# Performance work log

Hardware: AMD Instinct MI355X
Metric: run time of the kernel (lower is better)

Reference implementation:

```python
import math
import jax, jax.numpy as jnp
import numpy as np

B, NQ, NK, DIM, H, HD = 2, 1024, 2048, 1024, 16, 64


def setup_inputs() -> dict:
    key = jax.random.key(0)
    ks = jax.random.split(key, 12)
    s = 1.0 / math.sqrt(DIM)
    return {
        "q": jax.random.normal(ks[0], (B, NQ, DIM), jnp.float32),
        "k": jax.random.normal(ks[1], (B, NK, DIM), jnp.float32),
        "v": jax.random.normal(ks[2], (B, NK, DIM), jnp.float32),
        "distances": jax.random.uniform(ks[3], (B, NQ, NK), jnp.float32),
        "attn_mask": jax.random.bernoulli(ks[4], 0.5, (B, NQ, NK)),
        "key_padding_mask_q": jax.random.bernoulli(ks[5], 0.5, (B, NQ)),
        "key_padding_mask_k": jax.random.bernoulli(ks[6], 0.5, (B, NK)),
        "Wq": jax.random.normal(ks[7], (H * HD, DIM), jnp.float32) * s,
        "Wk": jax.random.normal(ks[8], (H * HD, DIM), jnp.float32) * s,
        "Wv": jax.random.normal(ks[9], (H * HD, DIM), jnp.float32) * s,
        "Wo": jax.random.normal(ks[10], (DIM, H * HD), jnp.float32) * s,
        "gate_alpha": jnp.float32(0.1),
    }


def reference(q, k, v, distances, attn_mask, key_padding_mask_q,
              key_padding_mask_k, Wq, Wk, Wv, Wo, gate_alpha):
    bsz, q_len, _ = q.shape
    k_len = k.shape[1]
    neg = jnp.finfo(q.dtype).min

    # projections -> (B, H, N, HD)
    qp = (q @ Wq.T).reshape(bsz, q_len, H, HD).transpose(0, 2, 1, 3)
    kp = (k @ Wk.T).reshape(bsz, k_len, H, HD).transpose(0, 2, 1, 3)
    vp = (v @ Wv.T).reshape(bsz, k_len, H, HD).transpose(0, 2, 1, 3)

    scores = jnp.einsum('bhqd,bhkd->bhqk', qp, kp) / math.sqrt(HD)
    scores = jnp.where(attn_mask[:, None, :, :], scores, neg)
    scores = jnp.where(key_padding_mask_k[:, None, None, :], scores, neg)

    attn = jax.nn.softmax(scores, axis=-1)  # (B,H,NQ,NK)

    # distance gating: mask, batch-mean normalize, exponential gate
    d = distances * attn_mask.astype(distances.dtype)
    d = d * key_padding_mask_k[:, None, :].astype(d.dtype)
    mean = d.sum(axis=(-1, -2)) / (q_len * k_len + 1e-6)
    mean = jnp.maximum(mean, 1e-6)[:, None, None]
    d = d / mean
    alpha = jax.nn.softplus(gate_alpha)
    gate = jnp.exp(-alpha * d)[:, None, :, :]  # (B,1,NQ,NK)

    w = attn * gate
    w = w / (w.sum(axis=-1, keepdims=True) + 1e-6)

    out = jnp.einsum('bhqk,bhkd->bhqd', w, vp)
    out = out.transpose(0, 2, 1, 3).reshape(bsz, q_len, H * HD)
    out = out * key_padding_mask_q[:, :, None].astype(out.dtype)
    return out @ Wo.T
```

## Files before the change

kernel.cpp:

```cpp
#include <hip/hip_runtime.h>
#include <hip/hip_bf16.h>
#include <cfloat>

#define B_   2
#define NQ_  1024
#define NK_  2048
#define H_   16
#define HD_  64
#define VPAD 2176
#define GPAD 2112

typedef float  floatx4 __attribute__((ext_vector_type(4)));
typedef __bf16 bf16x8  __attribute__((ext_vector_type(8)));
typedef __bf16 bf16x4  __attribute__((ext_vector_type(4)));

static __device__ __forceinline__ floatx4 mfma16(bf16x8 a, bf16x8 b, floatx4 c) {
    return __builtin_amdgcn_mfma_f32_16x16x32_bf16(a, b, c, 0, 0, 0);
}

static __device__ __forceinline__ void gl_lds(const __bf16* g, __bf16* lbase,
                                              int lane) {
#if __has_builtin(__builtin_amdgcn_global_load_lds)
    __builtin_amdgcn_global_load_lds(
        (const __attribute__((address_space(1))) void*)g,
        (__attribute__((address_space(3))) void*)lbase, 16, 0, 0);
#else
    *(bf16x8*)(lbase + lane * 8) = *(const bf16x8*)g;
#endif
}

struct CvtArgs {
    const float* src[7];
    __bf16*      dst[7];
};

__global__ __launch_bounds__(256) void cvt_mean_kernel(
    CvtArgs a, const float* __restrict__ dist, const int* __restrict__ amask,
    const int* __restrict__ kpmk, float* __restrict__ msum,
    __bf16* __restrict__ dmask)
{
    if (blockIdx.x >= 1792) {
        const int mb = blockIdx.x - 1792;
        const int b  = mb >> 9;
        const float* d  = dist  + (size_t)b * NQ_ * NK_;
        const int*   am = amask + (size_t)b * NQ_ * NK_;
        const int*   km = kpmk  + b * NK_;
        __bf16*      dm = dmask + (size_t)b * NQ_ * GPAD;
        const int base = (mb & 511) * 256 + threadIdx.x;
        float s = 0.f;
        #pragma unroll
        for (int j = 0; j < 4; j++) {
            const int i   = base + j * 131072;
            const int idx = i * 4;
            const int kk  = idx & (NK_ - 1);
            const int q   = i >> 9;
            float4 dv = *(const float4*)(d + idx);
            int4   mv = *(const int4*)(am + idx);
            int4   kv = *(const int4*)(km + kk);
            bf16x4 o;
            if (mv.x && kv.x) { s += dv.x; o[0] = (__bf16)dv.x; } else o[0] = (__bf16)3e38f;
            if (mv.y && kv.y) { s += dv.y; o[1] = (__bf16)dv.y; } else o[1] = (__bf16)3e38f;
            if (mv.z && kv.z) { s += dv.z; o[2] = (__bf16)dv.z; } else o[2] = (__bf16)3e38f;
            if (mv.w && kv.w) { s += dv.w; o[3] = (__bf16)dv.w; } else o[3] = (__bf16)3e38f;
            *(bf16x4*)&dm[(size_t)q * GPAD + kk] = o;
        }
        #pragma unroll
        for (int off = 32; off >= 1; off >>= 1) s += __shfl_down(s, off);
        __shared__ float wsum[4];
        if ((threadIdx.x & 63) == 0) wsum[threadIdx.x >> 6] = s;
        __syncthreads();
        if (threadIdx.x == 0)
            atomicAdd(&msum[b], wsum[0] + wsum[1] + wsum[2] + wsum[3]);
        return;
    }
    #pragma unroll
    for (int j = 0; j < 4; j++) {
        size_t r = (size_t)blockIdx.x * 1024 + j * 256 + threadIdx.x;
        int s;
        if (r < 262144)                  { s = 0; }
        else if ((r -= 262144) < 524288) { s = 1; }
        else if ((r -= 524288) < 524288) { s = 2; }
        else { r -= 524288; s = 3 + (int)(r >> 17); r &= 131071; }
        const float* sp = a.src[s] + r * 8;
        float4 f0 = *(const float4*)sp;
        float4 f1 = *(const float4*)(sp + 4);
        bf16x8 o;
        o[0] = (__bf16)f0.x; o[1] = (__bf16)f0.y; o[2] = (__bf16)f0.z; o[3] = (__bf16)f0.w;
        o[4] = (__bf16)f1.x; o[5] = (__bf16)f1.y; o[6] = (__bf16)f1.z; o[7] = (__bf16)f1.w;
        *(bf16x8*)(a.dst[s] + r * 8) = o;
    }
}

template <typename EPI>
static __device__ __forceinline__ void gemm128_core(
    const __bf16* __restrict__ A, const __bf16* __restrict__ Bw,
    int m0, int n0, __bf16* As, __bf16* Bs, EPI epi)
{
    const int t    = threadIdx.x;
    const int w    = t >> 6, lane = t & 63;
    const int lrow = lane & 15, quad = lane >> 4;
    const int lr   = lane >> 2, lc = lane & 3;

    floatx4 acc[4][4];
    #pragma unroll
    for (int mi = 0; mi < 4; mi++)
        #pragma unroll
        for (int ni = 0; ni < 4; ni++) acc[mi][ni] = floatx4{0.f, 0.f, 0.f, 0.f};

    const __bf16* ga = A  + (size_t)(m0 + w * 32 + lr) * 1024 + lc * 8;
    const __bf16* gb = Bw + (size_t)(n0 + w * 32 + lr) * 1024 + lc * 8;

    for (int k0 = 0; k0 < 1024; k0 += 64) {
        __syncthreads();
        #pragma unroll
        for (int h = 0; h < 2; h++) {
            gl_lds(ga + k0 + h * 32,             &As[h * 4096 + (w * 32) * 32],      lane);
            gl_lds(ga + k0 + h * 32 + 16 * 1024, &As[h * 4096 + (w * 32 + 16) * 32], lane);
            gl_lds(gb + k0 + h * 32,             &Bs[h * 4096 + (w * 32) * 32],      lane);
            gl_lds(gb + k0 + h * 32 + 16 * 1024, &Bs[h * 4096 + (w * 32 + 16) * 32], lane);
        }
        __syncthreads();

        #pragma unroll
        for (int h = 0; h < 2; h++) {
            bf16x8 af[4], bfr[4];
            #pragma unroll
            for (int mi = 0; mi < 4; mi++)
                af[mi] = *(const bf16x8*)
                    &As[h * 4096 + ((w & 1) * 64 + mi * 16 + lrow) * 32 + quad * 8];
            #pragma unroll
            for (int ni = 0; ni < 4; ni++)
                bfr[ni] = *(const bf16x8*)
                    &Bs[h * 4096 + ((w >> 1) * 64 + ni * 16 + lrow) * 32 + quad * 8];
            #pragma unroll
            for (int mi = 0; mi < 4; mi++)
                #pragma unroll
                for (int ni = 0; ni < 4; ni++)
                    acc[mi][ni] = mfma16(af[mi], bfr[ni], acc[mi][ni]);
        }
    }

    #pragma unroll
    for (int mi = 0; mi < 4; mi++)
        #pragma unroll
        for (int ni = 0; ni < 4; ni++)
            #pragma unroll
            for (int r = 0; r < 4; r++) {
                const int m = m0 + (w & 1) * 64 + mi * 16 + quad * 4 + r;
                const int n = n0 + (w >> 1) * 64 + ni * 16 + lrow;
                epi(m, n, acc[mi][ni][r]);
            }
}

__global__ __launch_bounds__(256) void proj_kernel(
    const __bf16* __restrict__ qb, const __bf16* __restrict__ kb,
    const __bf16* __restrict__ vb, const __bf16* __restrict__ wqb,
    const __bf16* __restrict__ wkb, const __bf16* __restrict__ wvb,
    __bf16* __restrict__ qp, __bf16* __restrict__ kp,
    __bf16* __restrict__ vpT)
{
    __shared__ alignas(16) __bf16 As[2 * 128 * 32];
    __shared__ alignas(16) __bf16 Bs[2 * 128 * 32];
    const int z = blockIdx.z;
    if (z == 0) {
        if ((int)blockIdx.x >= 16) return;
        gemm128_core(qb, wqb, blockIdx.x * 128, blockIdx.y * 128, As, Bs,
                     [&](int m, int n, float v) {
            const int b = m >> 10, q = m & 1023;
            const int h = n >> 6,  d = n & 63;
            qp[(((size_t)(b * 16 + h) * NQ_ + q) << 6) + d] = (__bf16)v;
        });
    } else if (z == 1) {
        gemm128_core(kb, wkb, blockIdx.x * 128, blockIdx.y * 128, As, Bs,
                     [&](int m, int n, float v) {
            const int b = m >> 11, key = m & 2047;
            const int h = n >> 6,  d = n & 63;
            kp[(((size_t)(b * 16 + h) * NK_ + key) << 6) + d] = (__bf16)v;
        });
    } else {
        gemm128_core(wvb, vb, blockIdx.y * 128, blockIdx.x * 128, As, Bs,
                     [&](int m, int n, float v) {
            const int h = m >> 6,  d = m & 63;
            const int b = n >> 11, key = n & 2047;
            vpT[((size_t)(b * 16 + h) * HD_ + d) * VPAD + key] = (__bf16)v;
        });
    }
}

__global__ __launch_bounds__(512) void oproj_kernel(
    const __bf16* __restrict__ A, const __bf16* __restrict__ W,
    float* __restrict__ Cout)
{
    __shared__ alignas(16) __bf16 As[2][64 * 32];
    __shared__ alignas(16) __bf16 Bs[2][128 * 32];
    const int t    = threadIdx.x;
    const int w    = t >> 6, lane = t & 63;
    const int lrow = lane & 15, quad = lane >> 4;
    const int lr   = lane >> 2, lc = lane & 3;
    const int m0 = blockIdx.x * 64, n0 = blockIdx.y * 128;
    const int wm = w & 1, wn = w >> 1;

    floatx4 acc[2][2];
    #pragma unroll
    for (int mi = 0; mi < 2; mi++)
        #pragma unroll
        for (int ni = 0; ni < 2; ni++) acc[mi][ni] = floatx4{0.f, 0.f, 0.f, 0.f};

    const __bf16* ga = A + (size_t)(m0 + (w & 3) * 16 + lr) * 1024 + lc * 8;
    const __bf16* gb = W + (size_t)(n0 + w * 16 + lr) * 1024 + lc * 8;

    for (int k0 = 0; k0 < 1024; k0 += 64) {
        __syncthreads();
        #pragma unroll
        for (int h = 0; h < 2; h++) {
            if (w < 4)
                gl_lds(ga + k0 + h * 32, &As[h][(w * 16) * 32], lane);
            gl_lds(gb + k0 + h * 32, &Bs[h][(w * 16) * 32], lane);
        }
        __syncthreads();

        #pragma unroll
        for (int h = 0; h < 2; h++) {
            bf16x8 af[2], bfr[2];
            #pragma unroll
            for (int mi = 0; mi < 2; mi++)
                af[mi] = *(const bf16x8*)
                    &As[h][(wm * 32 + mi * 16 + lrow) * 32 + quad * 8];
            #pragma unroll
            for (int ni = 0; ni < 2; ni++)
                bfr[ni] = *(const bf16x8*)
                    &Bs[h][(wn * 32 + ni * 16 + lrow) * 32 + quad * 8];
            #pragma unroll
            for (int mi = 0; mi < 2; mi++)
                #pragma unroll
                for (int ni = 0; ni < 2; ni++)
                    acc[mi][ni] = mfma16(af[mi], bfr[ni], acc[mi][ni]);
        }
    }

    #pragma unroll
    for (int mi = 0; mi < 2; mi++)
        #pragma unroll
        for (int ni = 0; ni < 2; ni++)
            #pragma unroll
            for (int r = 0; r < 4; r++) {
                const int m = m0 + wm * 32 + mi * 16 + quad * 4 + r;
                const int n = n0 + wn * 32 + ni * 16 + lrow;
                Cout[(size_t)m * 1024 + n] = acc[mi][ni][r];
            }
}

__global__ __launch_bounds__(256, 2) void attn_kernel(
    const __bf16* __restrict__ qp, const __bf16* __restrict__ kp,
    const __bf16* __restrict__ vpT, const __bf16* __restrict__ dmask,
    const float* __restrict__ msum, const float* __restrict__ galpha,
    float* __restrict__ Opart, float* __restrict__ Gpart)
{
    __shared__ __bf16 Ks[64 * 72];
    __shared__ __bf16 Vt[2][64 * 72];
    __shared__ __bf16 Ps[4][32 * 72];
    const int t    = threadIdx.x;
    const int w    = t >> 6, lane = t & 63;
    const int lrow = lane & 15, quad = lane >> 4;
    const int bid  = ((blockIdx.x & 7) << 6) | (blockIdx.x >> 3);
    const int qt   = bid & 7;
    const int bh   = (bid >> 3) & 31;
    const int z    = bid >> 8;
    const int b    = bh >> 4, h = bh & 15;
    const int q0   = qt * 128 + w * 32;
    const int kb0  = z * (NK_ / 2);
    const int NT   = NK_ / 128;

    const float mean  = fmaxf(msum[b] / ((float)(NQ_ * NK_) + 1e-6f), 1e-6f);
    const float alpha = log1pf(__expf(galpha[0]));
    const float cg    = -alpha / mean;

    bf16x8 qf0[2], qf1[2];
    #pragma unroll
    for (int g = 0; g < 2; g++) {
        const __bf16* qb = qp + ((size_t)bh * NQ_ + q0 + g * 16 + lrow) * HD_
                         + quad * 8;
        qf0[g] = *(const bf16x8*)qb;
        qf1[g] = *(const bf16x8*)(qb + 32);
    }

    const int srow0 = t >> 3,        sc0 = t & 7;
    const int srow1 = 32 + (t >> 3), sc1 = t & 7;
    const int so0 = srow0 * 72 + sc0 * 8;
    const int so1 = srow1 * 72 + sc1 * 8;
    const __bf16* Kg = kp  + ((size_t)bh * NK_ + kb0) * HD_;
    const __bf16* Vg = vpT + (size_t)bh * HD_ * VPAD + kb0;
    const __bf16* grow0 = dmask + ((size_t)b * NQ_ + q0 + lrow) * GPAD + kb0;
    const __bf16* grow1 = grow0 + (size_t)16 * GPAD;

    float G[2] = {0.f, 0.f};
    floatx4 O[2][4];
    #pragma unroll
    for (int g = 0; g < 2; g++)
        #pragma unroll
        for (int nb = 0; nb < 4; nb++) O[g][nb] = floatx4{0.f, 0.f, 0.f, 0.f};

    bf16x8 kr0, kr1, vr0, vr1;
    bf16x4 gr[2][4];
    auto loadt = [&](int kb) {
        kr0 = *(const bf16x8*)(Kg + (size_t)(kb + srow0) * HD_ + sc0 * 8);
        kr1 = *(const bf16x8*)(Kg + (size_t)(kb + srow1) * HD_ + sc1 * 8);
        vr0 = *(const bf16x8*)(Vg + (size_t)srow0 * VPAD + kb + sc0 * 8);
        vr1 = *(const bf16x8*)(Vg + (size_t)srow1 * VPAD + kb + sc1 * 8);
        #pragma unroll
        for (int c = 0; c < 4; c++) {
            gr[0][c] = *(const bf16x4*)(grow0 + kb + c * 16 + quad * 4);
            gr[1][c] = *(const bf16x4*)(grow1 + kb + c * 16 + quad * 4);
        }
    };
    loadt(0);

    for (int ib = 0; ib < NT; ib++) {
        const int kb  = ib * 64;
        const int cur = ib & 1;

        __syncthreads();
        *(bf16x8*)&Ks[so0]      = kr0;
        *(bf16x8*)&Ks[so1]      = kr1;
        *(bf16x8*)&Vt[cur][so0] = vr0;
        *(bf16x8*)&Vt[cur][so1] = vr1;
        __syncthreads();

        bf16x4 gcur[2][4];
        #pragma unroll
        for (int g = 0; g < 2; g++)
            #pragma unroll
            for (int c = 0; c < 4; c++) gcur[g][c] = gr[g][c];
        if (ib + 1 < NT) loadt(kb + 64);

        __builtin_amdgcn_s_setprio(1);
        floatx4 s4[2][4];
        #pragma unroll
        for (int c = 0; c < 4; c++) {
            bf16x8 kf0 = *(const bf16x8*)&Ks[(c * 16 + lrow) * 72 + quad * 8];
            bf16x8 kf1 = *(const bf16x8*)&Ks[(c * 16 + lrow) * 72 + 32 + quad * 8];
            #pragma unroll
            for (int g = 0; g < 2; g++) {
                floatx4 a = floatx4{0.f, 0.f, 0.f, 0.f};
                a = mfma16(kf0, qf0[g], a);
                a = mfma16(kf1, qf1[g], a);
                s4[g][c] = a;
            }
        }

        if (ib > 0) {
            const int prv = cur ^ 1;
            bf16x8 pf0[2], pf1[2];
            #pragma unroll
            for (int g = 0; g < 2; g++) {
                pf0[g] = *(const bf16x8*)&Ps[w][(g * 16 + lrow) * 72 + quad * 8];
                pf1[g] = *(const bf16x8*)&Ps[w][(g * 16 + lrow) * 72 + 32 + quad * 8];
            }
            #pragma unroll
            for (int nb = 0; nb < 4; nb++) {
                bf16x8 vf0 = *(const bf16x8*)
                    &Vt[prv][(nb * 16 + lrow) * 72 + quad * 8];
                bf16x8 vf1 = *(const bf16x8*)
                    &Vt[prv][(nb * 16 + lrow) * 72 + 32 + quad * 8];
                #pragma unroll
                for (int g = 0; g < 2; g++) {
                    O[g][nb] = mfma16(pf0[g], vf0, O[g][nb]);
                    O[g][nb] = mfma16(pf1[g], vf1, O[g][nb]);
                }
            }
        }
        __builtin_amdgcn_s_setprio(0);

        #pragma unroll
        for (int g = 0; g < 2; g++)
            #pragma unroll
            for (int c = 0; c < 4; c++) {
                const float e0 = __expf(fmaf(s4[g][c][0], 0.125f, cg * (float)gcur[g][c][0]));
                const float e1 = __expf(fmaf(s4[g][c][1], 0.125f, cg * (float)gcur[g][c][1]));
                const float e2 = __expf(fmaf(s4[g][c][2], 0.125f, cg * (float)gcur[g][c][2]));
                const float e3 = __expf(fmaf(s4[g][c][3], 0.125f, cg * (float)gcur[g][c][3]));
                G[g] += (e0 + e1) + (e2 + e3);
                bf16x4 pk;
                pk[0] = (__bf16)e0; pk[1] = (__bf16)e1;
                pk[2] = (__bf16)e2; pk[3] = (__bf16)e3;
                *(bf16x4*)&Ps[w][(g * 16 + lrow) * 72 + c * 16 + quad * 4] = pk;
            }
    }

    {
        const int prv = (NT - 1) & 1;
        bf16x8 pf0[2], pf1[2];
        #pragma unroll
        for (int g = 0; g < 2; g++) {
            pf0[g] = *(const bf16x8*)&Ps[w][(g * 16 + lrow) * 72 + quad * 8];
            pf1[g] = *(const bf16x8*)&Ps[w][(g * 16 + lrow) * 72 + 32 + quad * 8];
        }
        #pragma unroll
        for (int nb = 0; nb < 4; nb++) {
            bf16x8 vf0 = *(const bf16x8*)&Vt[prv][(nb * 16 + lrow) * 72 + quad * 8];
            bf16x8 vf1 = *(const bf16x8*)&Vt[prv][(nb * 16 + lrow) * 72 + 32 + quad * 8];
            #pragma unroll
            for (int g = 0; g < 2; g++) {
                O[g][nb] = mfma16(pf0[g], vf0, O[g][nb]);
                O[g][nb] = mfma16(pf1[g], vf1, O[g][nb]);
            }
        }
    }

    #pragma unroll
    for (int g = 0; g < 2; g++) {
        G[g] += __shfl_xor(G[g], 16);
        G[g] += __shfl_xor(G[g], 32);
    }

    #pragma unroll
    for (int g = 0; g < 2; g++) {
        float* Op = Opart + (size_t)z * (B_ * NQ_ * 1024)
                          + ((size_t)b * NQ_ + q0 + g * 16) * 1024 + h * HD_;
        #pragma unroll
        for (int r = 0; r < 4; r++) {
            const int qr = quad * 4 + r;
            #pragma unroll
            for (int nb = 0; nb < 4; nb++)
                Op[(size_t)qr * 1024 + nb * 16 + lrow] = O[g][nb][r];
        }
        if (lane < 16)
            Gpart[(size_t)z * (32 * 1024) + bh * 1024 + q0 + g * 16 + lane] = G[g];
    }
}

__global__ __launch_bounds__(256) void combine_kernel(
    const float* __restrict__ Opart, const float* __restrict__ Gpart,
    const int* __restrict__ kpmq, __bf16* __restrict__ attnout)
{
    const int idx = blockIdx.x * 256 + threadIdx.x;
    const int m   = idx >> 8;
    const int c4  = (idx & 255) * 4;
    const int b   = m >> 10, q = m & 1023;
    const int h   = c4 >> 6;
    const float g = Gpart[(b * 16 + h) * 1024 + q]
                  + Gpart[32 * 1024 + (b * 16 + h) * 1024 + q];
    const float f = kpmq[b * NQ_ + q] ? 1.f / (g + 1e-30f) : 0.f;
    const float4 o0 = *(const float4*)(Opart + (size_t)m * 1024 + c4);
    const float4 o1 = *(const float4*)(Opart + (size_t)(B_ * NQ_) * 1024
                                              + (size_t)m * 1024 + c4);
    bf16x4 r;
    r[0] = (__bf16)((o0.x + o1.x) * f);
    r[1] = (__bf16)((o0.y + o1.y) * f);
    r[2] = (__bf16)((o0.z + o1.z) * f);
    r[3] = (__bf16)((o0.w + o1.w) * f);
    *(bf16x4*)&attnout[(size_t)m * 1024 + c4] = r;
}

extern "C" void kernel_launch(void* const* d_in, const int* in_sizes, int n_in,
                              void* d_out, int out_size, void* d_ws,
                              size_t ws_size, hipStream_t stream)
{
    const float* q      = (const float*)d_in[0];
    const float* k      = (const float*)d_in[1];
    const float* v      = (const float*)d_in[2];
    const float* dist   = (const float*)d_in[3];
    const int*   amask  = (const int*)d_in[4];
    const int*   kpmq   = (const int*)d_in[5];
    const int*   kpmk   = (const int*)d_in[6];
    const float* Wq     = (const float*)d_in[7];
    const float* Wk     = (const float*)d_in[8];
    const float* Wv     = (const float*)d_in[9];
    const float* Wo     = (const float*)d_in[10];
    const float* galpha = (const float*)d_in[11];

    char* p = (char*)d_ws;
    float*  msum = (float*)p;                 p += 256;
    __bf16* qb   = (__bf16*)p;                p += (size_t)2097152 * 2;
    __bf16* kb   = (__bf16*)p;                p += (size_t)4194304 * 2;
    __bf16* vb   = (__bf16*)p;                p += (size_t)4194304 * 2;
    __bf16* wqb  = (__bf16*)p;                p += (size_t)1048576 * 2;
    __bf16* wkb  = (__bf16*)p;                p += (size_t)1048576 * 2;
    __bf16* wvb  = (__bf16*)p;                p += (size_t)1048576 * 2;
    __bf16* wob  = (__bf16*)p;                p += (size_t)1048576 * 2;
    __bf16* qp   = (__bf16*)p;                p += (size_t)2097152 * 2;
    __bf16* kpb  = (__bf16*)p;                p += (size_t)4194304 * 2;
    __bf16* vpT  = (__bf16*)p;                p += (size_t)32 * 64 * VPAD * 2;
    __bf16* dmask = (__bf16*)p;               p += (size_t)2048 * GPAD * 2;
    __bf16* attnout = (__bf16*)p;             p += (size_t)2097152 * 2;

    float* Opart = (float*)kb;
    float* Gpart = (float*)qb;

    CvtArgs ca;
    ca.src[0] = q;  ca.src[1] = k;  ca.src[2] = v;
    ca.src[3] = Wq; ca.src[4] = Wk; ca.src[5] = Wv; ca.src[6] = Wo;
    ca.dst[0] = qb;  ca.dst[1] = kb;  ca.dst[2] = vb;
    ca.dst[3] = wqb; ca.dst[4] = wkb; ca.dst[5] = wvb; ca.dst[6] = wob;

    hipMemsetAsync(msum, 0, 256, stream);
    cvt_mean_kernel<<<2816, 256, 0, stream>>>(ca, dist, amask, kpmk, msum,
                                              dmask);
    proj_kernel<<<dim3(32, 8, 3), 256, 0, stream>>>(qb, kb, vb, wqb, wkb, wvb,
                                                    qp, kpb, vpT);
    attn_kernel<<<512, 256, 0, stream>>>(qp, kpb, vpT, dmask,
                                         msum, galpha, Opart, Gpart);
    combine_kernel<<<2048, 256, 0, stream>>>(Opart, Gpart, kpmq, attnout);
    oproj_kernel<<<dim3(32, 8), 512, 0, stream>>>(attnout, wob, (float*)d_out);
}
```

Before: 249.2 us.

## Fuse fp32-to-bf16 activation conversion into projection GEMM loads

The separate conversion of the q, k and v activations to bf16 is removed from the preprocessing kernel. The projection GEMM now reads fp32 activations through registers, converts them to bf16 and writes them into LDS, with a one-step register prefetch of the next k-tile. This drops a full write and re-read of the bf16 activation copies. In exchange the GEMM reads twice as many bytes for the activation operand and does the conversion work inside its main loop, which may slow the GEMM itself.

```diff
diff --git a/kernel.cpp b/kernel.cpp
--- a/kernel.cpp
+++ b/kernel.cpp
@@ -39,8 +39,8 @@
     const int* __restrict__ kpmk, float* __restrict__ msum,
     __bf16* __restrict__ dmask)
 {
-    if (blockIdx.x >= 1792) {
-        const int mb = blockIdx.x - 1792;
+    if (blockIdx.x >= 512) {
+        const int mb = blockIdx.x - 512;
         const int b  = mb >> 9;
         const float* d  = dist  + (size_t)b * NQ_ * NK_;
         const int*   am = amask + (size_t)b * NQ_ * NK_;
@@ -76,11 +76,8 @@
     #pragma unroll
     for (int j = 0; j < 4; j++) {
         size_t r = (size_t)blockIdx.x * 1024 + j * 256 + threadIdx.x;
-        int s;
-        if (r < 262144)                  { s = 0; }
-        else if ((r -= 262144) < 524288) { s = 1; }
-        else if ((r -= 524288) < 524288) { s = 2; }
-        else { r -= 524288; s = 3 + (int)(r >> 17); r &= 131071; }
+        const int s = 3 + (int)(r >> 17);
+        r &= 131071;
         const float* sp = a.src[s] + r * 8;
         float4 f0 = *(const float4*)sp;
         float4 f1 = *(const float4*)(sp + 4);
@@ -91,15 +88,16 @@
     }
 }
 
-template <typename EPI>
-static __device__ __forceinline__ void gemm128_core(
-    const __bf16* __restrict__ A, const __bf16* __restrict__ Bw,
+template <bool AF32, typename EPI>
+static __device__ __forceinline__ void gemm128c_core(
+    const float* __restrict__ Fsrc, const __bf16* __restrict__ Bsrc,
     int m0, int n0, __bf16* As, __bf16* Bs, EPI epi)
 {
     const int t    = threadIdx.x;
     const int w    = t >> 6, lane = t & 63;
     const int lrow = lane & 15, quad = lane >> 4;
     const int lr   = lane >> 2, lc = lane & 3;
+    const int frow = t >> 1, fc16 = (t & 1) * 16;
 
     floatx4 acc[4][4];
     #pragma unroll
@@ -107,19 +105,47 @@
         #pragma unroll
         for (int ni = 0; ni < 4; ni++) acc[mi][ni] = floatx4{0.f, 0.f, 0.f, 0.f};
 
-    const __bf16* ga = A  + (size_t)(m0 + w * 32 + lr) * 1024 + lc * 8;
-    const __bf16* gb = Bw + (size_t)(n0 + w * 32 + lr) * 1024 + lc * 8;
-
+    const float*  gf  = Fsrc + (size_t)((AF32 ? m0 : n0) + frow) * 1024 + fc16;
+    const __bf16* gbb = Bsrc + (size_t)((AF32 ? n0 : m0) + w * 32 + lr) * 1024 + lc * 8;
+    __bf16* Fls = AF32 ? As : Bs;
+    __bf16* Bls = AF32 ? Bs : As;
+
+    float4 fr[2][4];
+    auto issueF = [&](int k0) {
+        #pragma unroll
+        for (int h = 0; h < 2; h++)
+            #pragma unroll
+            for (int j = 0; j < 4; j++)
+                fr[h][j] = *(const float4*)(gf + k0 + h * 32 + j * 4);
+    };
+    auto writeF = [&]() {
+        #pragma unroll
+        for (int h = 0; h < 2; h++) {
+            bf16x8 o0, o1;
+            o0[0] = (__bf16)fr[h][0].x; o0[1] = (__bf16)fr[h][0].y;
+            o0[2] = (__bf16)fr[h][0].z; o0[3] = (__bf16)fr[h][0].w;
+            o0[4] = (__bf16)fr[h][1].x; o0[5] = (__bf16)fr[h][1].y;
+            o0[6] = (__bf16)fr[h][1].z; o0[7] = (__bf16)fr[h][1].w;
+            o1[0] = (__bf16)fr[h][2].x; o1[1] = (__bf16)fr[h][2].y;
+            o1[2] = (__bf16)fr[h][2].z; o1[3] = (__bf16)fr[h][2].w;
+            o1[4] = (__bf16)fr[h][3].x; o1[5] = (__bf16)fr[h][3].y;
+            o1[6] = (__bf16)fr[h][3].z; o1[7] = (__bf16)fr[h][3].w;
+            *(bf16x8*)&Fls[h * 4096 + frow * 32 + fc16]     = o0;
+            *(bf16x8*)&Fls[h * 4096 + frow * 32 + fc16 + 8] = o1;
+        }
+    };
+
+    issueF(0);
     for (int k0 = 0; k0 < 1024; k0 += 64) {
         __syncthreads();
+        writeF();
         #pragma unroll
         for (int h = 0; h < 2; h++) {
-            gl_lds(ga + k0 + h * 32,             &As[h * 4096 + (w * 32) * 32],      lane);
-            gl_lds(ga + k0 + h * 32 + 16 * 1024, &As[h * 4096 + (w * 32 + 16) * 32], lane);
-            gl_lds(gb + k0 + h * 32,             &Bs[h * 4096 + (w * 32) * 32],      lane);
-            gl_lds(gb + k0 + h * 32 + 16 * 1024, &Bs[h * 4096 + (w * 32 + 16) * 32], lane);
-        }
-        __syncthreads();
+            gl_lds(gbb + k0 + h * 32,             &Bls[h * 4096 + (w * 32) * 32],      lane);
+            gl_lds(gbb + k0 + h * 32 + 16 * 1024, &Bls[h * 4096 + (w * 32 + 16) * 32], lane);
+        }
+        __syncthreads();
+        if (k0 + 64 < 1024) issueF(k0 + 64);
 
         #pragma unroll
         for (int h = 0; h < 2; h++) {
@@ -153,8 +179,8 @@
 }
 
 __global__ __launch_bounds__(256) void proj_kernel(
-    const __bf16* __restrict__ qb, const __bf16* __restrict__ kb,
-    const __bf16* __restrict__ vb, const __bf16* __restrict__ wqb,
+    const float* __restrict__ qf, const float* __restrict__ kf,
+    const float* __restrict__ vf, const __bf16* __restrict__ wqb,
     const __bf16* __restrict__ wkb, const __bf16* __restrict__ wvb,
     __bf16* __restrict__ qp, __bf16* __restrict__ kp,
     __bf16* __restrict__ vpT)
@@ -164,22 +190,22 @@
     const int z = blockIdx.z;
     if (z == 0) {
         if ((int)blockIdx.x >= 16) return;
-        gemm128_core(qb, wqb, blockIdx.x * 128, blockIdx.y * 128, As, Bs,
-                     [&](int m, int n, float v) {
+        gemm128c_core<true>(qf, wqb, blockIdx.x * 128, blockIdx.y * 128,
+                            As, Bs, [&](int m, int n, float v) {
             const int b = m >> 10, q = m & 1023;
             const int h = n >> 6,  d = n & 63;
             qp[(((size_t)(b * 16 + h) * NQ_ + q) << 6) + d] = (__bf16)v;
         });
     } else if (z == 1) {
-        gemm128_core(kb, wkb, blockIdx.x * 128, blockIdx.y * 128, As, Bs,
-                     [&](int m, int n, float v) {
+        gemm128c_core<true>(kf, wkb, blockIdx.x * 128, blockIdx.y * 128,
+                            As, Bs, [&](int m, int n, float v) {
             const int b = m >> 11, key = m & 2047;
             const int h = n >> 6,  d = n & 63;
             kp[(((size_t)(b * 16 + h) * NK_ + key) << 6) + d] = (__bf16)v;
         });
     } else {
-        gemm128_core(wvb, vb, blockIdx.y * 128, blockIdx.x * 128, As, Bs,
-                     [&](int m, int n, float v) {
+        gemm128c_core<false>(vf, wvb, blockIdx.y * 128, blockIdx.x * 128,
+                             As, Bs, [&](int m, int n, float v) {
             const int h = m >> 6,  d = m & 63;
             const int b = n >> 11, key = n & 2047;
             vpT[((size_t)(b * 16 + h) * HD_ + d) * VPAD + key] = (__bf16)v;
@@ -488,15 +514,15 @@
     float* Gpart = (float*)qb;
 
     CvtArgs ca;
-    ca.src[0] = q;  ca.src[1] = k;  ca.src[2] = v;
+    ca.src[0] = nullptr; ca.src[1] = nullptr; ca.src[2] = nullptr;
     ca.src[3] = Wq; ca.src[4] = Wk; ca.src[5] = Wv; ca.src[6] = Wo;
-    ca.dst[0] = qb;  ca.dst[1] = kb;  ca.dst[2] = vb;
+    ca.dst[0] = nullptr; ca.dst[1] = nullptr; ca.dst[2] = nullptr;
     ca.dst[3] = wqb; ca.dst[4] = wkb; ca.dst[5] = wvb; ca.dst[6] = wob;
 
     hipMemsetAsync(msum, 0, 256, stream);
-    cvt_mean_kernel<<<2816, 256, 0, stream>>>(ca, dist, amask, kpmk, msum,
+    cvt_mean_kernel<<<1536, 256, 0, stream>>>(ca, dist, amask, kpmk, msum,
                                               dmask);
-    proj_kernel<<<dim3(32, 8, 3), 256, 0, stream>>>(qb, kb, vb, wqb, wkb, wvb,
+    proj_kernel<<<dim3(32, 8, 3), 256, 0, stream>>>(q, k, v, wqb, wkb, wvb,
                                                     qp, kpb, vpT);
     attn_kernel<<<512, 256, 0, stream>>>(qp, kpb, vpT, dmask,
                                          msum, galpha, Opart, Gpart);
```

New measurement: 260.3 us. 4.4% more time.
